# Optimization experiments

Measured on AMD Instinct MI355X. Metric: run time of the kernel, lower is better.

The kernel has to match this reference:

```python
import jax, jax.numpy as jnp
import numpy as np
from jax import lax

N = 100000      # nodes
F_IN = 128      # dataset.num_features
H = 64          # hidden
E = 1600000     # edges
G = 1000        # graphs (equal-sized, contiguous)
PER = N // G    # nodes per graph = 100
K = 30          # sort-pool k
KS = 3          # conv1d kernel = num_layers


def setup_inputs() -> dict:
    key = jax.random.key(0)
    ks = jax.random.split(key, 20)
    lin = lambda k, i, o: (jax.random.normal(k, (i, o), jnp.float32) / np.sqrt(i)).astype(jnp.float32)
    return {
        "x": jax.random.normal(ks[0], (N, F_IN), jnp.float32),
        "src": jax.random.randint(ks[1], (E,), 0, N, dtype=jnp.int32),
        "dst": jax.random.randint(ks[2], (E,), 0, N, dtype=jnp.int32),
        "num_graphs": G,
        # SAGEConv 1: lin_l (aggr, with bias), lin_r (self, no bias)
        "wl1": lin(ks[3], F_IN, H), "wr1": lin(ks[4], F_IN, H), "b1": jnp.zeros((H,), jnp.float32),
        "wl2": lin(ks[5], H, H), "wr2": lin(ks[6], H, H), "b2": jnp.zeros((H,), jnp.float32),
        "wl3": lin(ks[7], H, H), "wr3": lin(ks[8], H, H), "b3": jnp.zeros((H,), jnp.float32),
        # Conv1d(hidden=64 -> 32, kernel=3): weight [O, I, K]
        "cw": (jax.random.normal(ks[9], (32, H, KS), jnp.float32) / np.sqrt(H * KS)).astype(jnp.float32),
        "cb": jnp.zeros((32,), jnp.float32),
        "w1": lin(ks[10], 32 * (K - KS + 1), H), "bb1": jnp.zeros((H,), jnp.float32),
        "w2": lin(ks[11], H, 1), "bb2": jnp.zeros((1,), jnp.float32),
    }


def _sage(x, src, dst, wl, wr, b, n):
    # PyG SAGEConv (mean aggr): lin_l(mean_{j->i} x_j) + lin_r(x_i)
    msum = jax.ops.segment_sum(x[src], dst, num_segments=n)           # [N, F]
    cnt = jax.ops.segment_sum(jnp.ones((src.shape[0],), x.dtype), dst, num_segments=n)
    mean = msum / jnp.maximum(cnt, 1.0)[:, None]
    return mean @ wl + b + x @ wr


def reference(x, src, dst, num_graphs, wl1, wr1, b1, wl2, wr2, b2, wl3, wr3, b3, cw, cb, w1, bb1, w2, bb2):
    n = x.shape[0]
    h = jax.nn.relu(_sage(x, src, dst, wl1, wr1, b1, n))
    h = jax.nn.relu(_sage(h, src, dst, wl2, wr2, b2, n))
    h = jax.nn.relu(_sage(h, src, dst, wl3, wr3, b3, n))
    # SortAggregation(k): per-graph, sort nodes by last feature channel (desc), keep top-k.
    # batch = contiguous equal-sized graphs -> dense reshape is exact.
    hg = h.reshape(num_graphs, PER, H)                                # [G, PER, H]
    order = jnp.argsort(-hg[:, :, -1], axis=1)[:, :K]                 # [G, K]
    topk = jnp.take_along_axis(hg, order[:, :, None], axis=1)         # [G, K, H]
    xc = jnp.transpose(topk, (0, 2, 1))                               # [G, H, K]
    y = lax.conv_general_dilated(xc, cw, (1,), 'VALID',
                                 dimension_numbers=('NCH', 'OIH', 'NCH'))
    y = jax.nn.relu(y + cb[None, :, None])                            # [G, 32, K-KS+1]
    y = y.reshape(num_graphs, -1)
    y = jax.nn.relu(y @ w1 + bb1)
    # dropout: eval mode -> identity
    return y @ w2 + bb2                                               # [G, 1]
```

## Files before the change

kernel.cpp:

```cpp
#include <hip/hip_runtime.h>

#define NN 100000
#define EE 1600000
#define GG 1000
#define PERG 100
#define KK 30
#define HH 64

#define NB 782
#define CAP 4096
#define CHB 4096
#define BUCKET_BLOCKS ((EE + CHB - 1) / CHB)
#define PROJ_BLOCKS ((NN + 127) / 128)
#define LAYER_BLOCKS ((NN + 63) / 64)

__device__ __forceinline__ void bucket_body(int bid, float* smem,
                                            const int* __restrict__ src,
                                            const int* __restrict__ dst,
                                            int* __restrict__ gcur,
                                            int* __restrict__ pairs) {
  int* lhist = (int*)smem;
  int* lbase = lhist + NB;
  int* lcur = lbase + NB;
  const int t = threadIdx.x;
  const int c0 = bid * CHB;
  const int c1 = min(c0 + CHB, EE);
  for (int b = t; b < NB; b += 256) {
    lhist[b] = 0;
    lcur[b] = 0;
  }
  __syncthreads();
  for (int e = c0 + t; e < c1; e += 256) atomicAdd(&lhist[dst[e] >> 7], 1);
  __syncthreads();
  for (int b = t; b < NB; b += 256) {
    int c = lhist[b];
    lbase[b] = c ? atomicAdd(&gcur[b], c) : 0;
  }
  __syncthreads();
  for (int e = c0 + t; e < c1; e += 256) {
    int d = dst[e];
    int b = d >> 7;
    int p = atomicAdd(&lcur[b], 1);
    pairs[b * CAP + lbase[b] + p] = (src[e] << 7) | (d & 127);
  }
}

template <int K>
__device__ __forceinline__ void proj_body(int bid, float* smem,
                                          const float* __restrict__ X,
                                          const float* __restrict__ WL,
                                          const float* __restrict__ WR,
                                          float* __restrict__ P,
                                          float* __restrict__ R) {
  constexpr int BM = 128, BK = 32, XSP = 40, WSP = 144;
  float* xs = smem;
  float* ws = smem + BM * XSP;
  const int t = threadIdx.x;
  const int row0 = bid * BM;
  const int tc = t & 15, tr = t >> 4;
  const int wcol = tc * 8 + (tc >> 2) * 4;

  float acc[8][8];
#pragma unroll
  for (int i = 0; i < 8; ++i)
#pragma unroll
    for (int j = 0; j < 8; ++j) acc[i][j] = 0.f;

  for (int k0 = 0; k0 < K; k0 += BK) {
    __syncthreads();
    for (int idx = t; idx < BM * 8; idx += 256) {
      int r = idx >> 3, c = idx & 7;
      int row = row0 + r;
      float4 v = make_float4(0.f, 0.f, 0.f, 0.f);
      if (row < NN) v = *reinterpret_cast<const float4*>(&X[(size_t)row * K + k0 + c * 4]);
      *reinterpret_cast<float4*>(&xs[r * XSP + c * 4]) = v;
    }
    for (int idx = t; idx < BK * 16; idx += 256) {
      int kr = idx >> 4, c4 = idx & 15;
      int gcl = c4 >> 1;
      int off = gcl * 8 + (gcl >> 2) * 4 + (c4 & 1) * 4;
      *reinterpret_cast<float4*>(&ws[kr * WSP + off]) =
          *reinterpret_cast<const float4*>(&WL[(k0 + kr) * 64 + c4 * 4]);
      int g2 = gcl + 8;
      int off2 = g2 * 8 + (g2 >> 2) * 4 + (c4 & 1) * 4;
      *reinterpret_cast<float4*>(&ws[kr * WSP + off2]) =
          *reinterpret_cast<const float4*>(&WR[(k0 + kr) * 64 + c4 * 4]);
    }
    __syncthreads();
    for (int kk4 = 0; kk4 < BK; kk4 += 4) {
      float4 a[8];
#pragma unroll
      for (int i = 0; i < 8; ++i)
        a[i] = *reinterpret_cast<const float4*>(&xs[(tr + 16 * i) * XSP + kk4]);
#pragma unroll
      for (int kk = 0; kk < 4; ++kk) {
        float4 b0 = *reinterpret_cast<const float4*>(&ws[(kk4 + kk) * WSP + wcol]);
        float4 b1 = *reinterpret_cast<const float4*>(&ws[(kk4 + kk) * WSP + wcol + 4]);
        float bv[8] = {b0.x, b0.y, b0.z, b0.w, b1.x, b1.y, b1.z, b1.w};
#pragma unroll
        for (int i = 0; i < 8; ++i) {
          float av = (kk == 0) ? a[i].x : (kk == 1) ? a[i].y : (kk == 2) ? a[i].z : a[i].w;
#pragma unroll
          for (int j = 0; j < 8; ++j) acc[i][j] = fmaf(av, bv[j], acc[i][j]);
        }
      }
    }
  }

  float* OUT = (tc < 8) ? P : R;
  int cb = (tc & 7) * 8;
#pragma unroll
  for (int i = 0; i < 8; ++i) {
    int row = row0 + tr + 16 * i;
    if (row < NN) {
      *reinterpret_cast<float4*>(&OUT[(size_t)row * 64 + cb]) =
          make_float4(acc[i][0], acc[i][1], acc[i][2], acc[i][3]);
      *reinterpret_cast<float4*>(&OUT[(size_t)row * 64 + cb + 4]) =
          make_float4(acc[i][4], acc[i][5], acc[i][6], acc[i][7]);
    }
  }
}

__global__ __launch_bounds__(256) void fused_bucket_proj(const int* __restrict__ src,
                                                         const int* __restrict__ dst,
                                                         int* __restrict__ gcur,
                                                         int* __restrict__ pairs,
                                                         const float* __restrict__ X,
                                                         const float* __restrict__ WL,
                                                         const float* __restrict__ WR,
                                                         float* __restrict__ P,
                                                         float* __restrict__ R) {
  __shared__ float smem[128 * 40 + 32 * 144];
  if (blockIdx.x < PROJ_BLOCKS)
    proj_body<128>(blockIdx.x, smem, X, WL, WR, P, R);
  else
    bucket_body(blockIdx.x - PROJ_BLOCKS, smem, src, dst, gcur, pairs);
}

__global__ __launch_bounds__(256) void csr_kernel(const int* __restrict__ gcur,
                                                  const int* __restrict__ pairs,
                                                  int* __restrict__ row_start,
                                                  int* __restrict__ cnt,
                                                  int* __restrict__ eidx) {
  __shared__ int vals[CAP];
  __shared__ int hist[128];
  __shared__ int offs[128];
  __shared__ int cur[128];
  __shared__ int red[4];
  const int b = blockIdx.x;
  const int t = threadIdx.x;
  int s = 0;
  for (int i = t; i < b; i += 256) s += gcur[i];
#pragma unroll
  for (int off = 32; off > 0; off >>= 1) s += __shfl_xor(s, off);
  if ((t & 63) == 0) red[t >> 6] = s;
  if (t < 128) {
    hist[t] = 0;
    cur[t] = 0;
  }
  __syncthreads();
  const int base = red[0] + red[1] + red[2] + red[3];
  const int nb = gcur[b];
  for (int i = t; i < nb; i += 256) {
    int v = pairs[b * CAP + i];
    vals[i] = v;
    atomicAdd(&hist[v & 127], 1);
  }
  __syncthreads();
  if (t < 128) {
    int ss = 0;
    for (int m = 0; m < t; ++m) ss += hist[m];
    offs[t] = ss;
    int node = b * 128 + t;
    if (node < NN) {
      row_start[node] = base + ss;
      cnt[node] = hist[t];
    }
  }
  __syncthreads();
  for (int i = t; i < nb; i += 256) {
    int v = vals[i];
    int ld = v & 127;
    int p = atomicAdd(&cur[ld], 1);
    eidx[base + offs[ld] + p] = v >> 7;
  }
}

__global__ __launch_bounds__(256) void agg_kernel(const float* __restrict__ P,
                                                  const float* __restrict__ R,
                                                  const float* __restrict__ bias,
                                                  const int* __restrict__ row_start,
                                                  const int* __restrict__ cnt,
                                                  const int* __restrict__ eidx,
                                                  float* __restrict__ h,
                                                  float* __restrict__ keys) {
  const int wv = (blockIdx.x * 256 + threadIdx.x) >> 6;
  const int lane = threadIdx.x & 63;
  const int q = lane >> 4;
  const int ql = lane & 15;
  const int node = wv * 4 + q;
  if (node >= NN) return;
  const int base = row_start[node];
  const int deg = cnt[node];
  float4 acc = make_float4(0.f, 0.f, 0.f, 0.f);

  for (int e0 = 0; e0 < deg; e0 += 16) {
    const int rem = deg - e0;
    const int ii = (ql < rem) ? ql : (rem - 1);
    int idx = eidx[base + e0 + ii];
#pragma unroll
    for (int j = 0; j < 16; ++j) {
      const int sj = __shfl(idx, (lane & 48) | j);
      const float wj = (j < rem) ? 1.f : 0.f;
      const float4 vj = *reinterpret_cast<const float4*>(&P[(size_t)sj * 64 + ql * 4]);
      acc.x = fmaf(wj, vj.x, acc.x);
      acc.y = fmaf(wj, vj.y, acc.y);
      acc.z = fmaf(wj, vj.z, acc.z);
      acc.w = fmaf(wj, vj.w, acc.w);
    }
  }

  const float dv = fmaxf((float)deg, 1.0f);
  float4 r4 = *reinterpret_cast<const float4*>(&R[(size_t)node * 64 + ql * 4]);
  float4 b4 = *reinterpret_cast<const float4*>(&bias[ql * 4]);
  float4 o;
  o.x = fmaxf(acc.x / dv + b4.x + r4.x, 0.f);
  o.y = fmaxf(acc.y / dv + b4.y + r4.y, 0.f);
  o.z = fmaxf(acc.z / dv + b4.z + r4.z, 0.f);
  o.w = fmaxf(acc.w / dv + b4.w + r4.w, 0.f);
  *reinterpret_cast<float4*>(&h[(size_t)node * 64 + ql * 4]) = o;
  if (keys != nullptr && ql == 15) keys[node] = o.w;
}

__global__ __launch_bounds__(256) void layer_kernel(const float* __restrict__ P,
                                                    const float* __restrict__ R,
                                                    const float* __restrict__ bias,
                                                    const int* __restrict__ row_start,
                                                    const int* __restrict__ cnt,
                                                    const int* __restrict__ eidx,
                                                    const float* __restrict__ WL,
                                                    const float* __restrict__ WR,
                                                    float* __restrict__ Pout,
                                                    float* __restrict__ Rout) {
  __shared__ float hs[64 * 68];
  const int t = threadIdx.x;
  const int lane = t & 63;
  const int qd = t >> 4;
  const int ql = t & 15;
  const int row0 = blockIdx.x * 64;

  for (int p = 0; p < 4; ++p) {
    const int r = qd + 16 * p;
    const int node = row0 + r;
    float4 acc = make_float4(0.f, 0.f, 0.f, 0.f);
    if (node < NN) {
      const int base = row_start[node];
      const int deg = cnt[node];
      for (int e0 = 0; e0 < deg; e0 += 16) {
        const int rem = deg - e0;
        const int ii = (ql < rem) ? ql : (rem - 1);
        int idx = eidx[base + e0 + ii];
#pragma unroll
        for (int j = 0; j < 16; ++j) {
          const int sj = __shfl(idx, (lane & 48) | j);
          const float wj = (j < rem) ? 1.f : 0.f;
          const float4 vj = *reinterpret_cast<const float4*>(&P[(size_t)sj * 64 + ql * 4]);
          acc.x = fmaf(wj, vj.x, acc.x);
          acc.y = fmaf(wj, vj.y, acc.y);
          acc.z = fmaf(wj, vj.z, acc.z);
          acc.w = fmaf(wj, vj.w, acc.w);
        }
      }
      const float dv = fmaxf((float)deg, 1.0f);
      const float4 r4 = *reinterpret_cast<const float4*>(&R[(size_t)node * 64 + ql * 4]);
      const float4 b4 = *reinterpret_cast<const float4*>(&bias[ql * 4]);
      acc.x = fmaxf(acc.x / dv + b4.x + r4.x, 0.f);
      acc.y = fmaxf(acc.y / dv + b4.y + r4.y, 0.f);
      acc.z = fmaxf(acc.z / dv + b4.z + r4.z, 0.f);
      acc.w = fmaxf(acc.w / dv + b4.w + r4.w, 0.f);
    }
    *reinterpret_cast<float4*>(&hs[r * 68 + ql * 4]) = acc;
  }
  __syncthreads();

  const int tc = t & 15, tr = t >> 4;
  const float* WB = (tc < 8) ? WL : WR;
  const int wcolg = (tc & 7) * 8;

  float acc[4][8];
#pragma unroll
  for (int i = 0; i < 4; ++i)
#pragma unroll
    for (int j = 0; j < 8; ++j) acc[i][j] = 0.f;

  for (int kk4 = 0; kk4 < 64; kk4 += 4) {
    float4 a[4];
#pragma unroll
    for (int i = 0; i < 4; ++i)
      a[i] = *reinterpret_cast<const float4*>(&hs[(tr + 16 * i) * 68 + kk4]);
#pragma unroll
    for (int kk = 0; kk < 4; ++kk) {
      float4 b0 = *reinterpret_cast<const float4*>(&WB[(kk4 + kk) * 64 + wcolg]);
      float4 b1 = *reinterpret_cast<const float4*>(&WB[(kk4 + kk) * 64 + wcolg + 4]);
      float bv[8] = {b0.x, b0.y, b0.z, b0.w, b1.x, b1.y, b1.z, b1.w};
#pragma unroll
      for (int i = 0; i < 4; ++i) {
        float av = (kk == 0) ? a[i].x : (kk == 1) ? a[i].y : (kk == 2) ? a[i].z : a[i].w;
#pragma unroll
        for (int j = 0; j < 8; ++j) acc[i][j] = fmaf(av, bv[j], acc[i][j]);
      }
    }
  }

  float* OUT = (tc < 8) ? Pout : Rout;
  const int cb = (tc & 7) * 8;
#pragma unroll
  for (int i = 0; i < 4; ++i) {
    int row = row0 + tr + 16 * i;
    if (row < NN) {
      *reinterpret_cast<float4*>(&OUT[(size_t)row * 64 + cb]) =
          make_float4(acc[i][0], acc[i][1], acc[i][2], acc[i][3]);
      *reinterpret_cast<float4*>(&OUT[(size_t)row * 64 + cb + 4]) =
          make_float4(acc[i][4], acc[i][5], acc[i][6], acc[i][7]);
    }
  }
}

__global__ __launch_bounds__(256) void head_kernel(const float* __restrict__ h,
                                                   const float* __restrict__ keysArr,
                                                   const float* __restrict__ cw,
                                                   const float* __restrict__ cb,
                                                   const float* __restrict__ w1,
                                                   const float* __restrict__ bb1,
                                                   const float* __restrict__ w2,
                                                   const float* __restrict__ bb2,
                                                   float* __restrict__ out) {
  __shared__ float key[PERG];
  __shared__ int sel[KK];
  __shared__ float feat[34 * 65];
  __shared__ float cwT[192 * 33];
  __shared__ float z[896];
  __shared__ float psum[256];
  const int g = blockIdx.x;
  const int t = threadIdx.x;

  for (int idx = t; idx < 32 * 192; idx += 256) {
    int o = idx / 192, k = idx % 192;
    cwT[k * 33 + o] = cw[idx];
  }
  if (t < PERG) key[t] = keysArr[g * PERG + t];
  __syncthreads();

  if (t < PERG) {
    float kv = key[t];
    int r = 0;
    for (int m = 0; m < PERG; ++m) {
      float km = key[m];
      r += (int)((km > kv) || (km == kv && m < t));
    }
    if (r < KK) sel[r] = t;
  }
  __syncthreads();

  for (int idx = t; idx < KK * HH; idx += 256) {
    int r = idx >> 6, f = idx & 63;
    feat[r * 65 + f] = h[(size_t)(g * PERG + sel[r]) * HH + f];
  }
  __syncthreads();

  {
    const int o = t & 31;
    const int pg = t >> 5;
    float zacc[4] = {0.f, 0.f, 0.f, 0.f};
    int i = 0, tt = 0;
    for (int k = 0; k < 192; ++k) {
      float c = cwT[k * 33 + o];
#pragma unroll
      for (int j = 0; j < 4; ++j) {
        int p = pg + 8 * j;
        zacc[j] = fmaf(c, feat[(p + tt) * 65 + i], zacc[j]);
      }
      if (++tt == 3) {
        tt = 0;
        ++i;
      }
    }
    float cbo = cb[o];
#pragma unroll
    for (int j = 0; j < 4; ++j) {
      int p = pg + 8 * j;
      if (p < 28) z[o * 28 + p] = fmaxf(zacc[j] + cbo, 0.f);
    }
  }
  __syncthreads();

  {
    const int hh = t & 63;
    const int quarter = t >> 6;
    const int q0 = quarter * 224;
    float acc = 0.f;
    for (int q = 0; q < 224; ++q)
      acc = fmaf(z[q0 + q], w1[(size_t)(q0 + q) * 64 + hh], acc);
    psum[t] = acc;
  }
  __syncthreads();

  if (t < 64) {
    float o1 = fmaxf(bb1[t] + psum[t] + psum[t + 64] + psum[t + 128] + psum[t + 192], 0.f);
    float v = o1 * w2[t];
#pragma unroll
    for (int off = 32; off > 0; off >>= 1) v += __shfl_down(v, off);
    if (t == 0) out[g] = v + bb2[0];
  }
}

extern "C" void kernel_launch(void* const* d_in, const int* in_sizes, int n_in,
                              void* d_out, int out_size, void* d_ws, size_t ws_size,
                              hipStream_t stream) {
  const float* x = (const float*)d_in[0];
  const int* src = (const int*)d_in[1];
  const int* dst = (const int*)d_in[2];
  const float* wl1 = (const float*)d_in[4];
  const float* wr1 = (const float*)d_in[5];
  const float* b1 = (const float*)d_in[6];
  const float* wl2 = (const float*)d_in[7];
  const float* wr2 = (const float*)d_in[8];
  const float* b2 = (const float*)d_in[9];
  const float* wl3 = (const float*)d_in[10];
  const float* wr3 = (const float*)d_in[11];
  const float* b3 = (const float*)d_in[12];
  const float* cw = (const float*)d_in[13];
  const float* cb = (const float*)d_in[14];
  const float* w1 = (const float*)d_in[15];
  const float* bb1 = (const float*)d_in[16];
  const float* w2 = (const float*)d_in[17];
  const float* bb2 = (const float*)d_in[18];
  float* out = (float*)d_out;

  char* w = (char*)d_ws;
  auto carve = [&](size_t bytes) {
    char* p = w;
    w += (bytes + 255) & ~(size_t)255;
    return p;
  };
  int* row_start = (int*)carve((size_t)NN * 4);
  int* cnt = (int*)carve((size_t)NN * 4);
  int* eidx = (int*)carve((size_t)EE * 4);
  float* P = (float*)carve((size_t)NN * 64 * 4);
  float* R = (float*)carve((size_t)NN * 64 * 4);
  float* hbuf = (float*)carve((size_t)NN * 64 * 4);
  float* R2 = (float*)carve((size_t)NN * 64 * 4);
  float* keys = (float*)carve((size_t)NN * 4);
  int* gcur = (int*)carve((size_t)NB * 4);
  int* pairs = (int*)hbuf;
  float* P2 = hbuf;

  hipMemsetAsync(gcur, 0, (size_t)NB * 4, stream);
  fused_bucket_proj<<<BUCKET_BLOCKS + PROJ_BLOCKS, 256, 0, stream>>>(
      src, dst, gcur, pairs, x, wl1, wr1, P, R);
  csr_kernel<<<NB, 256, 0, stream>>>(gcur, pairs, row_start, cnt, eidx);

  layer_kernel<<<LAYER_BLOCKS, 256, 0, stream>>>(P, R, b1, row_start, cnt, eidx,
                                                 wl2, wr2, P2, R2);
  layer_kernel<<<LAYER_BLOCKS, 256, 0, stream>>>(P2, R2, b2, row_start, cnt, eidx,
                                                 wl3, wr3, P, R);
  const int aggGrid = (NN + 15) / 16;
  agg_kernel<<<aggGrid, 256, 0, stream>>>(P, R, b3, row_start, cnt, eidx, hbuf, keys);
  head_kernel<<<GG, 256, 0, stream>>>(hbuf, keys, cw, cb, w1, bb1, w2, bb2, out);
}
```

Measured before the change: 487.4 us.

## Compute only sort keys for all nodes, aggregate full features for top-k only

The final full 64-channel aggregation over all nodes is replaced by a scalar key-only aggregation (the last channel of the projected features), followed by a per-graph kernel that selects the top-k nodes and aggregates full features only for those 30 of 100 nodes per graph. This removes about 70% of the last layer's gather traffic, at the cost of an extra kernel launch and a scattered per-thread key gather. The projection shared-memory padding is also reduced from 40 to 36, which may change bank-conflict behaviour.

```diff
diff --git a/kernel.cpp b/kernel.cpp
--- a/kernel.cpp
+++ b/kernel.cpp
@@ -52,7 +52,7 @@
                                           const float* __restrict__ WR,
                                           float* __restrict__ P,
                                           float* __restrict__ R) {
-  constexpr int BM = 128, BK = 32, XSP = 40, WSP = 144;
+  constexpr int BM = 128, BK = 32, XSP = 36, WSP = 144;
   float* xs = smem;
   float* ws = smem + BM * XSP;
   const int t = threadIdx.x;
@@ -130,7 +130,7 @@
                                                          const float* __restrict__ WR,
                                                          float* __restrict__ P,
                                                          float* __restrict__ R) {
-  __shared__ float smem[128 * 40 + 32 * 144];
+  __shared__ float smem[128 * 36 + 32 * 144];
   if (blockIdx.x < PROJ_BLOCKS)
     proj_body<128>(blockIdx.x, smem, X, WL, WR, P, R);
   else
@@ -186,52 +186,6 @@
   }
 }
 
-__global__ __launch_bounds__(256) void agg_kernel(const float* __restrict__ P,
-                                                  const float* __restrict__ R,
-                                                  const float* __restrict__ bias,
-                                                  const int* __restrict__ row_start,
-                                                  const int* __restrict__ cnt,
-                                                  const int* __restrict__ eidx,
-                                                  float* __restrict__ h,
-                                                  float* __restrict__ keys) {
-  const int wv = (blockIdx.x * 256 + threadIdx.x) >> 6;
-  const int lane = threadIdx.x & 63;
-  const int q = lane >> 4;
-  const int ql = lane & 15;
-  const int node = wv * 4 + q;
-  if (node >= NN) return;
-  const int base = row_start[node];
-  const int deg = cnt[node];
-  float4 acc = make_float4(0.f, 0.f, 0.f, 0.f);
-
-  for (int e0 = 0; e0 < deg; e0 += 16) {
-    const int rem = deg - e0;
-    const int ii = (ql < rem) ? ql : (rem - 1);
-    int idx = eidx[base + e0 + ii];
-#pragma unroll
-    for (int j = 0; j < 16; ++j) {
-      const int sj = __shfl(idx, (lane & 48) | j);
-      const float wj = (j < rem) ? 1.f : 0.f;
-      const float4 vj = *reinterpret_cast<const float4*>(&P[(size_t)sj * 64 + ql * 4]);
-      acc.x = fmaf(wj, vj.x, acc.x);
-      acc.y = fmaf(wj, vj.y, acc.y);
-      acc.z = fmaf(wj, vj.z, acc.z);
-      acc.w = fmaf(wj, vj.w, acc.w);
-    }
-  }
-
-  const float dv = fmaxf((float)deg, 1.0f);
-  float4 r4 = *reinterpret_cast<const float4*>(&R[(size_t)node * 64 + ql * 4]);
-  float4 b4 = *reinterpret_cast<const float4*>(&bias[ql * 4]);
-  float4 o;
-  o.x = fmaxf(acc.x / dv + b4.x + r4.x, 0.f);
-  o.y = fmaxf(acc.y / dv + b4.y + r4.y, 0.f);
-  o.z = fmaxf(acc.z / dv + b4.z + r4.z, 0.f);
-  o.w = fmaxf(acc.w / dv + b4.w + r4.w, 0.f);
-  *reinterpret_cast<float4*>(&h[(size_t)node * 64 + ql * 4]) = o;
-  if (keys != nullptr && ql == 15) keys[node] = o.w;
-}
-
 __global__ __launch_bounds__(256) void layer_kernel(const float* __restrict__ P,
                                                     const float* __restrict__ R,
                                                     const float* __restrict__ bias,
@@ -241,7 +195,9 @@
                                                     const float* __restrict__ WL,
                                                     const float* __restrict__ WR,
                                                     float* __restrict__ Pout,
-                                                    float* __restrict__ Rout) {
+                                                    float* __restrict__ Rout,
+                                                    float* __restrict__ keyP,
+                                                    float* __restrict__ keyR) {
   __shared__ float hs[64 * 68];
   const int t = threadIdx.x;
   const int lane = t & 63;
@@ -322,12 +278,103 @@
           make_float4(acc[i][0], acc[i][1], acc[i][2], acc[i][3]);
       *reinterpret_cast<float4*>(&OUT[(size_t)row * 64 + cb + 4]) =
           make_float4(acc[i][4], acc[i][5], acc[i][6], acc[i][7]);
-    }
-  }
-}
-
-__global__ __launch_bounds__(256) void head_kernel(const float* __restrict__ h,
-                                                   const float* __restrict__ keysArr,
+      if (keyP != nullptr && tc == 7) keyP[row] = acc[i][7];
+      if (keyR != nullptr && tc == 15) keyR[row] = acc[i][7];
+    }
+  }
+}
+
+__global__ __launch_bounds__(256) void keys_kernel(const float* __restrict__ keyP,
+                                                   const float* __restrict__ keyR,
+                                                   const float* __restrict__ b3,
+                                                   const int* __restrict__ row_start,
+                                                   const int* __restrict__ cnt,
+                                                   const int* __restrict__ eidx,
+                                                   float* __restrict__ keys) {
+  const int node = blockIdx.x * 256 + threadIdx.x;
+  if (node >= NN) return;
+  const int base = row_start[node];
+  const int deg = cnt[node];
+  float s = 0.f;
+  for (int e0 = 0; e0 < deg; e0 += 16) {
+    const int rem = deg - e0;
+    int id[16];
+#pragma unroll
+    for (int k = 0; k < 16; ++k) id[k] = eidx[base + e0 + ((k < rem) ? k : rem - 1)];
+    float v[16];
+#pragma unroll
+    for (int k = 0; k < 16; ++k) v[k] = keyP[id[k]];
+#pragma unroll
+    for (int k = 0; k < 16; ++k) s += (k < rem) ? v[k] : 0.f;
+  }
+  const float dv = fmaxf((float)deg, 1.f);
+  keys[node] = fmaxf(s / dv + b3[63] + keyR[node], 0.f);
+}
+
+__global__ __launch_bounds__(256) void sel_gather(const float* __restrict__ P,
+                                                  const float* __restrict__ R,
+                                                  const float* __restrict__ bias,
+                                                  const float* __restrict__ keysArr,
+                                                  const int* __restrict__ row_start,
+                                                  const int* __restrict__ cnt,
+                                                  const int* __restrict__ eidx,
+                                                  float* __restrict__ feat) {
+  __shared__ float key[PERG];
+  __shared__ int sel[32];
+  const int g = blockIdx.x;
+  const int t = threadIdx.x;
+  if (t < PERG) key[t] = keysArr[g * PERG + t];
+  __syncthreads();
+  if (t < PERG) {
+    float kv = key[t];
+    int r = 0;
+    for (int m = 0; m < PERG; ++m) {
+      float km = key[m];
+      r += (int)((km > kv) || (km == kv && m < t));
+    }
+    if (r < KK) sel[r] = t;
+  }
+  __syncthreads();
+
+  const int lane = t & 63;
+  const int qd = t >> 4;
+  const int ql = t & 15;
+  for (int p = 0; p < 2; ++p) {
+    const int r = qd + 16 * p;
+    if (r < KK) {
+      const int node = g * PERG + sel[r];
+      const int base = row_start[node];
+      const int deg = cnt[node];
+      float4 acc = make_float4(0.f, 0.f, 0.f, 0.f);
+      for (int e0 = 0; e0 < deg; e0 += 16) {
+        const int rem = deg - e0;
+        const int ii = (ql < rem) ? ql : (rem - 1);
+        int idx = eidx[base + e0 + ii];
+#pragma unroll
+        for (int j = 0; j < 16; ++j) {
+          const int sj = __shfl(idx, (lane & 48) | j);
+          const float wj = (j < rem) ? 1.f : 0.f;
+          const float4 vj = *reinterpret_cast<const float4*>(&P[(size_t)sj * 64 + ql * 4]);
+          acc.x = fmaf(wj, vj.x, acc.x);
+          acc.y = fmaf(wj, vj.y, acc.y);
+          acc.z = fmaf(wj, vj.z, acc.z);
+          acc.w = fmaf(wj, vj.w, acc.w);
+        }
+      }
+      const float dv = fmaxf((float)deg, 1.0f);
+      const float4 r4 = *reinterpret_cast<const float4*>(&R[(size_t)node * 64 + ql * 4]);
+      const float4 b4 = *reinterpret_cast<const float4*>(&bias[ql * 4]);
+      float4 o;
+      o.x = fmaxf(acc.x / dv + b4.x + r4.x, 0.f);
+      o.y = fmaxf(acc.y / dv + b4.y + r4.y, 0.f);
+      o.z = fmaxf(acc.z / dv + b4.z + r4.z, 0.f);
+      o.w = fmaxf(acc.w / dv + b4.w + r4.w, 0.f);
+      *reinterpret_cast<float4*>(&feat[((size_t)g * KK + r) * 64 + ql * 4]) = o;
+    }
+  }
+}
+
+__global__ __launch_bounds__(256) void head_kernel(const float* __restrict__ gfeat,
                                                    const float* __restrict__ cw,
                                                    const float* __restrict__ cb,
                                                    const float* __restrict__ w1,
@@ -335,8 +382,6 @@
                                                    const float* __restrict__ w2,
                                                    const float* __restrict__ bb2,
                                                    float* __restrict__ out) {
-  __shared__ float key[PERG];
-  __shared__ int sel[KK];
   __shared__ float feat[34 * 65];
   __shared__ float cwT[192 * 33];
   __shared__ float z[896];
@@ -348,23 +393,9 @@
     int o = idx / 192, k = idx % 192;
     cwT[k * 33 + o] = cw[idx];
   }
-  if (t < PERG) key[t] = keysArr[g * PERG + t];
-  __syncthreads();
-
-  if (t < PERG) {
-    float kv = key[t];
-    int r = 0;
-    for (int m = 0; m < PERG; ++m) {
-      float km = key[m];
-      r += (int)((km > kv) || (km == kv && m < t));
-    }
-    if (r < KK) sel[r] = t;
-  }
-  __syncthreads();
-
   for (int idx = t; idx < KK * HH; idx += 256) {
     int r = idx >> 6, f = idx & 63;
-    feat[r * 65 + f] = h[(size_t)(g * PERG + sel[r]) * HH + f];
+    feat[r * 65 + f] = gfeat[((size_t)g * KK + r) * 64 + f];
   }
   __syncthreads();
 
@@ -448,12 +479,14 @@
   int* eidx = (int*)carve((size_t)EE * 4);
   float* P = (float*)carve((size_t)NN * 64 * 4);
   float* R = (float*)carve((size_t)NN * 64 * 4);
-  float* hbuf = (float*)carve((size_t)NN * 64 * 4);
+  float* P2 = (float*)carve((size_t)NN * 64 * 4);
   float* R2 = (float*)carve((size_t)NN * 64 * 4);
   float* keys = (float*)carve((size_t)NN * 4);
+  float* keyP = (float*)carve((size_t)NN * 4);
+  float* keyR = (float*)carve((size_t)NN * 4);
+  float* feat = (float*)carve((size_t)GG * KK * HH * 4);
   int* gcur = (int*)carve((size_t)NB * 4);
-  int* pairs = (int*)hbuf;
-  float* P2 = hbuf;
+  int* pairs = (int*)P2;
 
   hipMemsetAsync(gcur, 0, (size_t)NB * 4, stream);
   fused_bucket_proj<<<BUCKET_BLOCKS + PROJ_BLOCKS, 256, 0, stream>>>(
@@ -461,10 +494,11 @@
   csr_kernel<<<NB, 256, 0, stream>>>(gcur, pairs, row_start, cnt, eidx);
 
   layer_kernel<<<LAYER_BLOCKS, 256, 0, stream>>>(P, R, b1, row_start, cnt, eidx,
-                                                 wl2, wr2, P2, R2);
+                                                 wl2, wr2, P2, R2, nullptr, nullptr);
   layer_kernel<<<LAYER_BLOCKS, 256, 0, stream>>>(P2, R2, b2, row_start, cnt, eidx,
-                                                 wl3, wr3, P, R);
-  const int aggGrid = (NN + 15) / 16;
-  agg_kernel<<<aggGrid, 256, 0, stream>>>(P, R, b3, row_start, cnt, eidx, hbuf, keys);
-  head_kernel<<<GG, 256, 0, stream>>>(hbuf, keys, cw, cb, w1, bb1, w2, bb2, out);
-}
+                                                 wl3, wr3, P, R, keyP, keyR);
+  keys_kernel<<<(NN + 255) / 256, 256, 0, stream>>>(keyP, keyR, b3, row_start, cnt,
+                                                    eidx, keys);
+  sel_gather<<<GG, 256, 0, stream>>>(P, R, b3, keys, row_start, cnt, eidx, feat);
+  head_kernel<<<GG, 256, 0, stream>>>(feat, cw, cb, w1, bb1, w2, bb2, out);
+}
```

New measurement: 452.8 us. 7.1% less time.
